# Optimization experiments

Measured on AMD Instinct MI355X. Metric: run time of the kernel, lower is better.

## Reference

```python
import jax, jax.numpy as jnp
import numpy as np


def _avgpool2(x):
    # 2x2 average pool, stride 2 (NCHW)
    n, c, h, w = x.shape
    return x.reshape(n, c, h // 2, 2, w // 2, 2).mean(axis=(3, 5))


def setup_inputs() -> dict:
    key = jax.random.key(0)
    k1, k2, k3, k4 = jax.random.split(key, 4)
    N, H, W = 32, 512, 512
    N2 = H // 4
    eps = 1e-4  # keep probabilities strictly inside (0,1) for BCE
    logits = jax.random.uniform(k1, (N, 1, H, W), jnp.float32, eps, 1.0 - eps)
    labels = jax.random.uniform(k2, (N, 1, H, W), jnp.float32, eps, 1.0 - eps)
    v_attention = jax.random.uniform(k3, (N, 1, N2, N2), jnp.float32)
    h_attention = jax.random.uniform(k4, (N, 1, N2, N2), jnp.float32)
    return {"logits": logits, "labels": labels,
            "v_attention": v_attention, "h_attention": h_attention}


def reference(logits, labels, v_attention, h_attention):
    N = labels.shape[0]
    smooth = 1.0

    # --- BCE over all elements ---
    p = logits.reshape(-1)
    y = labels.reshape(-1)
    bceloss = -jnp.mean(y * jnp.log(p) + (1.0 - y) * jnp.log(1.0 - p))

    # --- Dice on thresholded logits ---
    masks = (logits > 0.4).astype(logits.dtype)
    input_flat = masks.reshape(N, -1)
    target_flat = labels.reshape(N, -1)
    intersection = (input_flat * target_flat).sum(axis=1)
    dice = 2.0 * (intersection + smooth) / (input_flat.sum(axis=1) + target_flat.sum(axis=1) + smooth)
    diceloss = 1.0 - dice.sum() / N

    # --- Per-sample 3-way Pearson-style correlation ---
    N1 = v_attention.shape[0]
    attent_labels = _avgpool2(_avgpool2(labels))          # [N,1,H/4,W/4]
    v = v_attention.reshape(N1, -1)                        # [N1, N2*N2]
    h = h_attention.reshape(N1, -1)
    l = attent_labels.reshape(N1, -1)
    vc = v - v.mean(axis=1, keepdims=True)
    hc = h - h.mean(axis=1, keepdims=True)
    lc = l - l.mean(axis=1, keepdims=True)
    num = (vc * hc * lc).sum(axis=1)
    den = jnp.sqrt((vc * vc).sum(axis=1) * (hc * hc).sum(axis=1) * (lc * lc).sum(axis=1))
    cor_loss = -(num / den).sum() / N1

    return 0.2 * bceloss + 0.3 * diceloss + 0.5 * cor_loss
```

## Files before the change

### kernel.cpp

```cpp
#include <hip/hip_runtime.h>
#include <math.h>

#define NSAMP 32
#define HW 512
#define PW 128
#define NPOOL (PW * PW)
#define BPS 16
#define NBLOCKS (NSAMP * BPS)
#define PPT 4
#define NACC 14


__device__ __forceinline__ float wave_sum_dpp(float x) {
#define DPP_ADD(ctrl)                                                         \
    x += __int_as_float(__builtin_amdgcn_update_dpp(                          \
        0, __float_as_int(x), (ctrl), 0xf, 0xf, true));
    DPP_ADD(0x111)
    DPP_ADD(0x112)
    DPP_ADD(0x114)
    DPP_ADD(0x118)
    DPP_ADD(0x142)
    DPP_ADD(0x143)
#undef DPP_ADD
    return x;
}

__global__ __launch_bounds__(256, 2) void covloss_main(
    const float* __restrict__ logits, const float* __restrict__ labels,
    const float* __restrict__ v_att,  const float* __restrict__ h_att,
    float* __restrict__ part)
{
    const int bid   = blockIdx.x;
    const int n     = bid >> 4;
    const int local = bid & 15;
    const int pbase = local * (PPT * 256);

    const float* lg = logits + (size_t)n * HW * HW;
    const float* lb = labels + (size_t)n * HW * HW;
    const float* va = v_att + (size_t)n * NPOOL;
    const float* ha = h_att + (size_t)n * NPOOL;

    float bce = 0.f, inter = 0.f, ysum = 0.f;
    unsigned long long cnt_u = 0;
    float S_v = 0.f, S_h = 0.f, S_l = 0.f;
    float S_vv = 0.f, S_hh = 0.f, S_ll = 0.f;
    float S_vh = 0.f, S_vl = 0.f, S_hl = 0.f, S_vhl = 0.f;

    float4 PA[4], YA[4]; float vA, hA;
    float4 PB[4], YB[4]; float vB, hB;
    float4 PC[4], YC[4]; float vC, hC;

#define LOADBUF(S, p) {                                                       \
    const int pidx = pbase + (p) * 256 + (int)threadIdx.x;                    \
    const int pr = pidx >> 7, pc = pidx & 127;                                \
    const float4* lg4 = (const float4*)(lg + (size_t)(4 * pr) * HW) + pc;     \
    const float4* lb4 = (const float4*)(lb + (size_t)(4 * pr) * HW) + pc;     \
    P##S[0] = lg4[0]; P##S[1] = lg4[HW / 4];                                  \
    P##S[2] = lg4[2 * (HW / 4)]; P##S[3] = lg4[3 * (HW / 4)];                 \
    Y##S[0] = lb4[0]; Y##S[1] = lb4[HW / 4];                                  \
    Y##S[2] = lb4[2 * (HW / 4)]; Y##S[3] = lb4[3 * (HW / 4)];                 \
    v##S = va[pidx]; h##S = ha[pidx]; }

#define COMPUTE(S) {                                                          \
    float lsum = 0.f;                                                         \
    _Pragma("unroll")                                                         \
    for (int i = 0; i < 4; ++i) {                                             \
        const float pv[4] = {P##S[i].x, P##S[i].y, P##S[i].z, P##S[i].w};     \
        const float yv[4] = {Y##S[i].x, Y##S[i].y, Y##S[i].z, Y##S[i].w};     \
        _Pragma("unroll")                                                     \
        for (int j = 0; j < 4; ++j) {                                         \
            const float pp = pv[j], y = yv[j];                                \
            bce = fmaf(y, __log2f(pp), bce);                                  \
            bce = fmaf(1.f - y, __log2f(1.f - pp), bce);                      \
            const bool m = pp > 0.4f;                                         \
            cnt_u += __popcll(__ballot(m));                                   \
            inter += m ? y : 0.f;                                             \
            lsum  += y;                                                       \
        }                                                                     \
    }                                                                         \
    ysum += lsum;                                                             \
    const float l = lsum * 0.0625f;                                           \
    const float v = v##S, h = h##S;                                           \
    S_v += v; S_h += h; S_l += l;                                             \
    S_vv = fmaf(v, v, S_vv); S_hh = fmaf(h, h, S_hh); S_ll = fmaf(l, l, S_ll);\
    const float vh = v * h;                                                   \
    S_vh += vh; S_vl = fmaf(v, l, S_vl); S_hl = fmaf(h, l, S_hl);             \
    S_vhl = fmaf(vh, l, S_vhl); }

    LOADBUF(A, 0)
    LOADBUF(B, 1)
    LOADBUF(C, 2)
    COMPUTE(A)
    LOADBUF(A, 3)
    COMPUTE(B)
    COMPUTE(C)
    COMPUTE(A)

#undef LOADBUF
#undef COMPUTE

    float vals[13] = { bce, inter, ysum,
                       S_v, S_h, S_l, S_vv, S_hh, S_ll,
                       S_vh, S_vl, S_hl, S_vhl };
#pragma unroll
    for (int k = 0; k < 13; ++k) vals[k] = wave_sum_dpp(vals[k]);

    __shared__ float sh[4][NACC];
    const int lane = threadIdx.x & 63, wv = threadIdx.x >> 6;
    if (lane == 63) {
        sh[wv][0] = vals[0];
        sh[wv][1] = (float)cnt_u;
        sh[wv][2] = vals[1];
        sh[wv][3] = vals[2];
#pragma unroll
        for (int k = 3; k < 13; ++k) sh[wv][k + 1] = vals[k];
    }
    __syncthreads();
    if (threadIdx.x < NACC) {
        part[(size_t)threadIdx.x * NBLOCKS + bid] =
            sh[0][threadIdx.x] + sh[1][threadIdx.x] + sh[2][threadIdx.x] + sh[3][threadIdx.x];
    }
}

__global__ __launch_bounds__(256) void covloss_finalize(
    const float* __restrict__ part, float* __restrict__ out)
{
    const int t = threadIdx.x;
    __shared__ double acc[NSAMP][NACC];

    for (int pair = t; pair < NSAMP * NACC; pair += 256) {
        const int s = pair / NACC, k = pair % NACC;
        const float4* p = (const float4*)(part + (size_t)k * NBLOCKS + s * BPS);
        double a = 0.0;
#pragma unroll
        for (int i = 0; i < 4; ++i) {
            const float4 q = p[i];
            a += (double)q.x + (double)q.y + (double)q.z + (double)q.w;
        }
        acc[s][k] = a;
    }
    __syncthreads();

    __shared__ double sb[NSAMP], sd[NSAMP], sc[NSAMP];
    if (t < NSAMP) {
        const double* a = acc[t];
        const double nn = (double)NPOOL;
        const double cvv = a[7] - a[4] * a[4] / nn;
        const double chh = a[8] - a[5] * a[5] / nn;
        const double cll = a[9] - a[6] * a[6] / nn;
        const double num = a[13]
            - (a[4] * a[12] + a[5] * a[11] + a[6] * a[10]) / nn
            + 2.0 * a[4] * a[5] * a[6] / (nn * nn);
        sc[t] = num / sqrt(cvv * chh * cll);
        sd[t] = 2.0 * (a[2] + 1.0) / (a[1] + a[3] + 1.0);
        sb[t] = a[0];
    }
    __syncthreads();
    if (t == 0) {
        double bces = 0.0, ds = 0.0, cs = 0.0;
#pragma unroll
        for (int i = 0; i < NSAMP; ++i) { bces += sb[i]; ds += sd[i]; cs += sc[i]; }
        const double bceloss = -(bces * M_LN2) / ((double)NSAMP * HW * HW);
        out[0] = (float)(0.2 * bceloss + 0.3 * (1.0 - ds / NSAMP) + 0.5 * (-cs / NSAMP));
    }
}

extern "C" void kernel_launch(void* const* d_in, const int* in_sizes, int n_in,
                              void* d_out, int out_size, void* d_ws, size_t ws_size,
                              hipStream_t stream) {
    const float* logits = (const float*)d_in[0];
    const float* labels = (const float*)d_in[1];
    const float* v_att  = (const float*)d_in[2];
    const float* h_att  = (const float*)d_in[3];
    float* out  = (float*)d_out;
    float* part = (float*)d_ws;

    covloss_main<<<NBLOCKS, 256, 0, stream>>>(logits, labels, v_att, h_att, part);
    covloss_finalize<<<1, 256, 0, stream>>>(part, out);
}
```

Before: 20.68 us.

## Fuse finalize into main kernel via last-block atomic counter

Merges the separate finalize kernel into the main reduction kernel. Each block publishes its partial sums with agent-scope atomic stores, then bumps a monotonically increasing global counter, and the last block to arrive performs the final double-precision reduction. This removes the second kernel launch and its inter-kernel gap. In exchange it adds atomics and a serialized tail in one block, and correctness depends on relaxed-ordering visibility and on the counter baseline read at kernel start.

```diff
diff --git a/kernel.cpp b/kernel.cpp
--- a/kernel.cpp
+++ b/kernel.cpp
@@ -25,11 +25,18 @@
     return x;
 }
 
-__global__ __launch_bounds__(256, 2) void covloss_main(
+__global__ __launch_bounds__(256, 2) void covloss_fused(
     const float* __restrict__ logits, const float* __restrict__ labels,
     const float* __restrict__ v_att,  const float* __restrict__ h_att,
-    float* __restrict__ part)
+    float* __restrict__ out, unsigned long long* __restrict__ ws)
 {
+    unsigned long long* counter = ws;
+    float* part = (float*)(ws + 8);
+
+    unsigned long long s0 = 0;
+    if (threadIdx.x == 0)
+        s0 = __hip_atomic_load(counter, __ATOMIC_RELAXED, __HIP_MEMORY_SCOPE_AGENT);
+
     const int bid   = blockIdx.x;
     const int n     = bid >> 4;
     const int local = bid & 15;
@@ -116,27 +123,34 @@
         for (int k = 3; k < 13; ++k) sh[wv][k + 1] = vals[k];
     }
     __syncthreads();
+
     if (threadIdx.x < NACC) {
-        part[(size_t)threadIdx.x * NBLOCKS + bid] =
-            sh[0][threadIdx.x] + sh[1][threadIdx.x] + sh[2][threadIdx.x] + sh[3][threadIdx.x];
+        const float p = sh[0][threadIdx.x] + sh[1][threadIdx.x] +
+                        sh[2][threadIdx.x] + sh[3][threadIdx.x];
+        __hip_atomic_store(&part[(size_t)threadIdx.x * NBLOCKS + bid], p,
+                           __ATOMIC_RELAXED, __HIP_MEMORY_SCOPE_AGENT);
     }
-}
 
-__global__ __launch_bounds__(256) void covloss_finalize(
-    const float* __restrict__ part, float* __restrict__ out)
-{
+    __shared__ int lastflag;
+    if (threadIdx.x == 0) {
+        __builtin_amdgcn_s_waitcnt(0);
+        const unsigned long long old = __hip_atomic_fetch_add(
+            counter, 1ULL, __ATOMIC_RELAXED, __HIP_MEMORY_SCOPE_AGENT);
+        lastflag = (old == s0 + (NBLOCKS - 1));
+    }
+    __syncthreads();
+    if (!lastflag) return;
+
     const int t = threadIdx.x;
     __shared__ double acc[NSAMP][NACC];
-
     for (int pair = t; pair < NSAMP * NACC; pair += 256) {
         const int s = pair / NACC, k = pair % NACC;
-        const float4* p = (const float4*)(part + (size_t)k * NBLOCKS + s * BPS);
+        const float* p = part + (size_t)k * NBLOCKS + s * BPS;
         double a = 0.0;
 #pragma unroll
-        for (int i = 0; i < 4; ++i) {
-            const float4 q = p[i];
-            a += (double)q.x + (double)q.y + (double)q.z + (double)q.w;
-        }
+        for (int i = 0; i < BPS; ++i)
+            a += (double)__hip_atomic_load(p + i, __ATOMIC_RELAXED,
+                                           __HIP_MEMORY_SCOPE_AGENT);
         acc[s][k] = a;
     }
     __syncthreads();
@@ -172,9 +186,8 @@
     const float* labels = (const float*)d_in[1];
     const float* v_att  = (const float*)d_in[2];
     const float* h_att  = (const float*)d_in[3];
-    float* out  = (float*)d_out;
-    float* part = (float*)d_ws;
+    float* out = (float*)d_out;
+    unsigned long long* ws = (unsigned long long*)d_ws;
 
-    covloss_main<<<NBLOCKS, 256, 0, stream>>>(logits, labels, v_att, h_att, part);
-    covloss_finalize<<<1, 256, 0, stream>>>(part, out);
+    covloss_fused<<<NBLOCKS, 256, 0, stream>>>(logits, labels, v_att, h_att, out, ws);
 }
```

After: 26.16 us. +26.5%, slower.

## Stage logits/labels via direct global-to-LDS loads with double buffering

Applied to the files above, without the earlier changes.

Replaces the register triple-buffered float4 loads with asynchronous global_load_lds transfers into a 64KB double-buffered LDS area, synchronised per wave with explicit vmcnt waits. The aim is to cut register pressure and keep more loads in flight while compute runs on the other buffer. In exchange it uses 64KB of shared memory per block, which limits occupancy, and drops the 2-blocks launch bound. Correctness depends on the hand-counted waitcnt values and on each wave reading only its own LDS slice.

```diff
diff --git a/kernel.cpp b/kernel.cpp
--- a/kernel.cpp
+++ b/kernel.cpp
@@ -10,6 +10,16 @@
 #define PPT 4
 #define NACC 14
 
+
+#define AS1 __attribute__((address_space(1)))
+#define AS3 __attribute__((address_space(3)))
+
+__device__ __forceinline__ void g2l16(const float* g, float* l) {
+    __builtin_amdgcn_global_load_lds((const AS1 void*)g, (AS3 void*)l, 16, 0, 0);
+}
+
+#define FENCE()   do { asm volatile("" ::: "memory"); } while (0)
+#define WAITV(n)  do { asm volatile("s_waitcnt vmcnt(" #n ")" ::: "memory"); } while (0)
 
 __device__ __forceinline__ float wave_sum_dpp(float x) {
 #define DPP_ADD(ctrl)                                                         \
@@ -25,15 +35,19 @@
     return x;
 }
 
-__global__ __launch_bounds__(256, 2) void covloss_main(
+__global__ __launch_bounds__(256) void covloss_main(
     const float* __restrict__ logits, const float* __restrict__ labels,
     const float* __restrict__ v_att,  const float* __restrict__ h_att,
     float* __restrict__ part)
 {
+    __shared__ __align__(16) float lds[16384];
+
     const int bid   = blockIdx.x;
     const int n     = bid >> 4;
     const int local = bid & 15;
     const int pbase = local * (PPT * 256);
+    const int tid   = threadIdx.x;
+    const int wv    = tid >> 6, lane = tid & 63;
 
     const float* lg = logits + (size_t)n * HW * HW;
     const float* lb = labels + (size_t)n * HW * HW;
@@ -46,27 +60,29 @@
     float S_vv = 0.f, S_hh = 0.f, S_ll = 0.f;
     float S_vh = 0.f, S_vl = 0.f, S_hl = 0.f, S_vhl = 0.f;
 
-    float4 PA[4], YA[4]; float vA, hA;
-    float4 PB[4], YB[4]; float vB, hB;
-    float4 PC[4], YC[4]; float vC, hC;
-
-#define LOADBUF(S, p) {                                                       \
-    const int pidx = pbase + (p) * 256 + (int)threadIdx.x;                    \
+#define STAGE(b, p) do {                                                      \
+    const int pidx = pbase + (p) * 256 + tid;                                 \
     const int pr = pidx >> 7, pc = pidx & 127;                                \
-    const float4* lg4 = (const float4*)(lg + (size_t)(4 * pr) * HW) + pc;     \
-    const float4* lb4 = (const float4*)(lb + (size_t)(4 * pr) * HW) + pc;     \
-    P##S[0] = lg4[0]; P##S[1] = lg4[HW / 4];                                  \
-    P##S[2] = lg4[2 * (HW / 4)]; P##S[3] = lg4[3 * (HW / 4)];                 \
-    Y##S[0] = lb4[0]; Y##S[1] = lb4[HW / 4];                                  \
-    Y##S[2] = lb4[2 * (HW / 4)]; Y##S[3] = lb4[3 * (HW / 4)];                 \
-    v##S = va[pidx]; h##S = ha[pidx]; }
-
-#define COMPUTE(S) {                                                          \
+    const float* gl = lg + (size_t)(4 * pr) * HW + 4 * pc;                    \
+    const float* gy = lb + (size_t)(4 * pr) * HW + 4 * pc;                    \
+    float* dl = &lds[(b) * 8192 + wv * 1024];                                 \
+    float* dy = &lds[(b) * 8192 + 4096 + wv * 1024];                          \
+    g2l16(gl,          dl);        g2l16(gl + HW,     dl + 256);              \
+    g2l16(gl + 2 * HW, dl + 512);  g2l16(gl + 3 * HW, dl + 768);              \
+    g2l16(gy,          dy);        g2l16(gy + HW,     dy + 256);              \
+    g2l16(gy + 2 * HW, dy + 512);  g2l16(gy + 3 * HW, dy + 768);              \
+} while (0)
+
+#define COMPUTE(b, vS, hS) do {                                               \
+    const float4* Lp = (const float4*)&lds[(b) * 8192 + wv * 1024];           \
+    const float4* Yp = (const float4*)&lds[(b) * 8192 + 4096 + wv * 1024];    \
     float lsum = 0.f;                                                         \
     _Pragma("unroll")                                                         \
     for (int i = 0; i < 4; ++i) {                                             \
-        const float pv[4] = {P##S[i].x, P##S[i].y, P##S[i].z, P##S[i].w};     \
-        const float yv[4] = {Y##S[i].x, Y##S[i].y, Y##S[i].z, Y##S[i].w};     \
+        const float4 p4 = Lp[i * 64 + lane];                                  \
+        const float4 y4 = Yp[i * 64 + lane];                                  \
+        const float pv[4] = {p4.x, p4.y, p4.z, p4.w};                         \
+        const float yv[4] = {y4.x, y4.y, y4.z, y4.w};                         \
         _Pragma("unroll")                                                     \
         for (int j = 0; j < 4; ++j) {                                         \
             const float pp = pv[j], y = yv[j];                                \
@@ -80,23 +96,37 @@
     }                                                                         \
     ysum += lsum;                                                             \
     const float l = lsum * 0.0625f;                                           \
-    const float v = v##S, h = h##S;                                           \
-    S_v += v; S_h += h; S_l += l;                                             \
-    S_vv = fmaf(v, v, S_vv); S_hh = fmaf(h, h, S_hh); S_ll = fmaf(l, l, S_ll);\
-    const float vh = v * h;                                                   \
-    S_vh += vh; S_vl = fmaf(v, l, S_vl); S_hl = fmaf(h, l, S_hl);             \
-    S_vhl = fmaf(vh, l, S_vhl); }
-
-    LOADBUF(A, 0)
-    LOADBUF(B, 1)
-    LOADBUF(C, 2)
-    COMPUTE(A)
-    LOADBUF(A, 3)
-    COMPUTE(B)
-    COMPUTE(C)
-    COMPUTE(A)
-
-#undef LOADBUF
+    S_v += vS; S_h += hS; S_l += l;                                           \
+    S_vv = fmaf(vS, vS, S_vv); S_hh = fmaf(hS, hS, S_hh);                     \
+    S_ll = fmaf(l, l, S_ll);                                                  \
+    const float vh = vS * hS;                                                 \
+    S_vh += vh; S_vl = fmaf(vS, l, S_vl); S_hl = fmaf(hS, l, S_hl);           \
+    S_vhl = fmaf(vh, l, S_vhl);                                               \
+} while (0)
+
+    const int px0 = pbase + tid, px1 = px0 + 256, px2 = px0 + 512, px3 = px0 + 768;
+    const float v0 = va[px0], h0 = ha[px0];
+    const float v1 = va[px1], h1 = ha[px1];
+    const float v2 = va[px2], h2 = ha[px2];
+    const float v3 = va[px3], h3 = ha[px3];
+    FENCE();
+    STAGE(0, 0); FENCE();
+    STAGE(1, 1); FENCE();
+
+    WAITV(8);
+    COMPUTE(0, v0, h0);
+    FENCE();
+    STAGE(0, 2); FENCE();
+    WAITV(8);
+    COMPUTE(1, v1, h1);
+    FENCE();
+    STAGE(1, 3); FENCE();
+    WAITV(8);
+    COMPUTE(0, v2, h2);
+    WAITV(0);
+    COMPUTE(1, v3, h3);
+
+#undef STAGE
 #undef COMPUTE
 
     float vals[13] = { bce, inter, ysum,
@@ -106,7 +136,6 @@
     for (int k = 0; k < 13; ++k) vals[k] = wave_sum_dpp(vals[k]);
 
     __shared__ float sh[4][NACC];
-    const int lane = threadIdx.x & 63, wv = threadIdx.x >> 6;
     if (lane == 63) {
         sh[wv][0] = vals[0];
         sh[wv][1] = (float)cnt_u;
@@ -116,9 +145,9 @@
         for (int k = 3; k < 13; ++k) sh[wv][k + 1] = vals[k];
     }
     __syncthreads();
-    if (threadIdx.x < NACC) {
-        part[(size_t)threadIdx.x * NBLOCKS + bid] =
-            sh[0][threadIdx.x] + sh[1][threadIdx.x] + sh[2][threadIdx.x] + sh[3][threadIdx.x];
+    if (tid < NACC) {
+        part[(size_t)tid * NBLOCKS + bid] =
+            sh[0][tid] + sh[1][tid] + sh[2][tid] + sh[3][tid];
     }
 }
 
```

Result: slower. 22.40 us (+8.3%).
